# Kernel tuning notes

Hardware: AMD Instinct MI355X
Metric: run time of the kernel (lower is better)

Reference implementation:

```python
import jax, jax.numpy as jnp
import numpy as np

BN_EPS = 1e-5
NUM_GRAPHS = 64


def setup_inputs() -> dict:
    key = jax.random.key(0)
    ks = jax.random.split(key, 16)
    N, E, C_in, H, L, G = 100000, 1600000, 32, 64, 4, NUM_GRAPHS
    x = jax.random.normal(ks[0], (N, C_in), dtype=jnp.float32)
    edge_index = jax.random.randint(ks[1], (2, E), 0, N, dtype=jnp.int64)
    batch = jnp.sort(jax.random.randint(ks[2], (N,), 0, G, dtype=jnp.int64))
    s_in = 1.0 / np.sqrt(C_in)
    s_h = 1.0 / np.sqrt(H)
    s_2h = 1.0 / np.sqrt(2 * H)
    Win = jax.random.uniform(ks[3], (C_in, H), jnp.float32, -s_in, s_in)
    bin_ = jax.random.uniform(ks[4], (H,), jnp.float32, -s_in, s_in)
    W1s = jax.random.uniform(ks[5], (L, H, 2 * H), jnp.float32, -s_h, s_h)
    b1s = jax.random.uniform(ks[6], (L, 2 * H), jnp.float32, -s_h, s_h)
    gammas = jnp.ones((L, 2 * H), jnp.float32)
    betas = jnp.zeros((L, 2 * H), jnp.float32)
    W2s = jax.random.uniform(ks[7], (L, 2 * H, H), jnp.float32, -s_2h, s_2h)
    b2s = jax.random.uniform(ks[8], (L, H), jnp.float32, -s_2h, s_2h)
    epss = jnp.zeros((L,), jnp.float32)
    Wout = jax.random.uniform(ks[9], (H, 1), jnp.float32, -s_h, s_h)
    bout = jax.random.uniform(ks[10], (1,), jnp.float32, -s_h, s_h)
    return {"x": x, "edge_index": edge_index, "batch": batch, "Win": Win,
            "bin_": bin_, "W1s": W1s, "b1s": b1s, "gammas": gammas,
            "betas": betas, "W2s": W2s, "b2s": b2s, "epss": epss,
            "Wout": Wout, "bout": bout}


def _gin_layer(x, src, dst, W1, b1, gamma, beta, W2, b2, eps, n_nodes):
    # message: relu of source node features; aggregate: scatter-add at target
    agg = jax.ops.segment_sum(jax.nn.relu(x[src]), dst, num_segments=n_nodes)
    h = (1.0 + eps) * x + agg
    h = h @ W1 + b1
    mu = jnp.mean(h, axis=0)
    var = jnp.mean(jnp.square(h - mu), axis=0)  # biased, as in BatchNorm1d
    h = (h - mu) * jax.lax.rsqrt(var + BN_EPS) * gamma + beta
    h = jax.nn.relu(h)
    return h @ W2 + b2


def reference(x, edge_index, batch, Win, bin_, W1s, b1s, gammas, betas,
              W2s, b2s, epss, Wout, bout):
    N = x.shape[0]
    src, dst = edge_index[0], edge_index[1]
    x = x @ Win + bin_
    for l in range(W1s.shape[0]):
        x = x + _gin_layer(x, src, dst, W1s[l], b1s[l], gammas[l], betas[l],
                           W2s[l], b2s[l], epss[l], N)
    pooled = jax.ops.segment_sum(x, batch, num_segments=NUM_GRAPHS)  # [G, H]
    out = pooled @ Wout + bout
    return out.reshape(-1)
```

## Files before the change

### kernel.cpp

```cpp
#include <hip/hip_runtime.h>
#include <hip/hip_fp16.h>

#define H 64
#define CIN 32
#define TWOH 128
#define NGRAPH 64

#define BSH 7
#define BNODE 128
#define NBLK_PART 256
#define BCAP 32
#define MAXNB 2048
#define OCAP 65536

typedef unsigned short bfraw;
typedef short v8s __attribute__((ext_vector_type(8)));
typedef float v4f __attribute__((ext_vector_type(4)));

__device__ __forceinline__ float bf2f(bfraw u) {
    return __uint_as_float(((unsigned)u) << 16);
}
__device__ __forceinline__ bfraw f2bf(float f) {
    unsigned u = __float_as_uint(f);
    unsigned r = (u + 0x7fffu + ((u >> 16) & 1u)) >> 16;
    return (bfraw)r;
}
__device__ __forceinline__ void f2bf2(float f, bfraw& hi, bfraw& lo) {
    hi = f2bf(f);
    lo = f2bf(f - bf2f(hi));
}
__device__ __forceinline__ bfraw f2h(float f) {
    return __half_as_ushort(__float2half(f));
}
__device__ __forceinline__ __half2 u2h2(unsigned u) {
    union { unsigned u; __half2 h; } c; c.u = u; return c.h;
}

extern "C" __global__ void __launch_bounds__(256) k_input_gemm(
    const float* __restrict__ x, const float* __restrict__ Win,
    const float* __restrict__ bin, float* __restrict__ x0,
    bfraw* __restrict__ xh, int N)
{
    const int lane = threadIdx.x & 63;
    const int row = lane & 15;
    const int kg  = lane >> 4;
    v8s bhi[4], blo[4];
    #pragma unroll
    for (int ct = 0; ct < 4; ++ct) {
        v8s bh, bl;
        #pragma unroll
        for (int i = 0; i < 8; ++i) {
            const float w = Win[(kg * 8 + i) * H + ct * 16 + row];
            bfraw h, l; f2bf2(w, h, l);
            bh[i] = (short)h; bl[i] = (short)l;
        }
        bhi[ct] = bh; blo[ct] = bl;
    }
    float bcol[4];
    #pragma unroll
    for (int ct = 0; ct < 4; ++ct) bcol[ct] = bin[ct * 16 + row];

    const int wpb = blockDim.x >> 6;
    const int wid = blockIdx.x * wpb + (threadIdx.x >> 6);
    const int wstride = gridDim.x * wpb;
    const int tiles = (N + 15) >> 4;
    for (int t = wid; t < tiles; t += wstride) {
        const int tb = t << 4;
        int nA = tb + row; if (nA >= N) nA = N - 1;
        v8s ah, al;
        #pragma unroll
        for (int i = 0; i < 8; ++i) {
            const float v = x[(size_t)nA * CIN + kg * 8 + i];
            bfraw h, l; f2bf2(v, h, l);
            ah[i] = (short)h; al[i] = (short)l;
        }
        v4f c[4];
        #pragma unroll
        for (int ct = 0; ct < 4; ++ct) {
            v4f cc = (v4f){0.f, 0.f, 0.f, 0.f};
            cc = __builtin_amdgcn_mfma_f32_16x16x32_bf16(ah, bhi[ct], cc, 0, 0, 0);
            cc = __builtin_amdgcn_mfma_f32_16x16x32_bf16(ah, blo[ct], cc, 0, 0, 0);
            cc = __builtin_amdgcn_mfma_f32_16x16x32_bf16(al, bhi[ct], cc, 0, 0, 0);
            c[ct] = cc;
        }
        #pragma unroll
        for (int ct = 0; ct < 4; ++ct) {
            #pragma unroll
            for (int r = 0; r < 4; ++r) {
                const int node = tb + kg * 4 + r;
                if (node < N) {
                    const float v = c[ct][r] + bcol[ct];
                    const size_t idx = (size_t)node * H + ct * 16 + row;
                    x0[idx] = v;
                    xh[idx] = f2h(fmaxf(v, 0.f));
                }
            }
        }
    }
}

extern "C" __global__ void k_cvtw(const float* __restrict__ W1s,
    const float* __restrict__ W2s, bfraw* __restrict__ W1hi,
    bfraw* __restrict__ W1lo, bfraw* __restrict__ W2hi,
    bfraw* __restrict__ W2lo, int total)
{
    int i = blockIdx.x * blockDim.x + threadIdx.x;
    const int st = gridDim.x * blockDim.x;
    for (; i < total; i += st) {
        bfraw h, l;
        f2bf2(W1s[i], h, l); W1hi[i] = h; W1lo[i] = l;
        f2bf2(W2s[i], h, l); W2hi[i] = h; W2lo[i] = l;
    }
}

__device__ __forceinline__ void bput(int s, int d, unsigned* __restrict__ lcnt,
    unsigned* __restrict__ myTmp, unsigned* __restrict__ deg,
    int* __restrict__ oflow, unsigned* __restrict__ ocnt)
{
    const int b = d >> BSH;
    const unsigned pos = atomicAdd(&lcnt[b], 1u);
    if (pos < BCAP) {
        myTmp[b * BCAP + pos] = (unsigned)s | ((unsigned)(d & (BNODE - 1)) << 20);
    } else {
        const unsigned o = atomicAdd(ocnt, 1u);
        if (o < OCAP) {
            oflow[2 * o] = s; oflow[2 * o + 1] = d;
            atomicAdd(&deg[d], 1u);
        }
    }
}

extern "C" __global__ void __launch_bounds__(256) k_bucket(
    const int* __restrict__ src, const int* __restrict__ dst,
    unsigned* __restrict__ bcnt, unsigned* __restrict__ btmp,
    unsigned* __restrict__ deg, int* __restrict__ oflow,
    unsigned* __restrict__ ocnt, int E, int NBck)
{
    __shared__ unsigned lcnt[MAXNB];
    for (int i = threadIdx.x; i < NBck; i += blockDim.x) lcnt[i] = 0u;
    __syncthreads();
    unsigned* __restrict__ myTmp = btmp + (size_t)blockIdx.x * NBck * BCAP;
    const int tid0 = blockIdx.x * blockDim.x + threadIdx.x;
    const int st = gridDim.x * blockDim.x;
    const int E4 = E >> 2;
    const int4* s4 = (const int4*)src;
    const int4* d4 = (const int4*)dst;
    for (int j = tid0; j < E4; j += st) {
        const int4 sv = s4[j];
        const int4 dv = d4[j];
        bput(sv.x, dv.x, lcnt, myTmp, deg, oflow, ocnt);
        bput(sv.y, dv.y, lcnt, myTmp, deg, oflow, ocnt);
        bput(sv.z, dv.z, lcnt, myTmp, deg, oflow, ocnt);
        bput(sv.w, dv.w, lcnt, myTmp, deg, oflow, ocnt);
    }
    for (int j = (E4 << 2) + tid0; j < E; j += st)
        bput(src[j], dst[j], lcnt, myTmp, deg, oflow, ocnt);
    __syncthreads();
    unsigned* __restrict__ myCnt = bcnt + (size_t)blockIdx.x * NBck;
    for (int i = threadIdx.x; i < NBck; i += blockDim.x) {
        const unsigned c = lcnt[i];
        myCnt[i] = (c < BCAP) ? c : BCAP;
    }
}

extern "C" __global__ void __launch_bounds__(256) k_bhist(
    const unsigned* __restrict__ bcnt, const unsigned* __restrict__ btmp,
    unsigned* __restrict__ deg, int N, int NBck)
{
    __shared__ unsigned hist[BNODE];
    const int b = blockIdx.x;
    for (int i = threadIdx.x; i < BNODE; i += blockDim.x) hist[i] = 0u;
    __syncthreads();
    for (int blk = threadIdx.x; blk < NBLK_PART; blk += blockDim.x) {
        const unsigned cnt = bcnt[(size_t)blk * NBck + b];
        const unsigned* p = btmp + ((size_t)blk * NBck + b) * BCAP;
        for (unsigned j = 0; j < cnt; ++j)
            atomicAdd(&hist[p[j] >> 20], 1u);
    }
    __syncthreads();
    const int base = b << BSH;
    for (int i = threadIdx.x; i < BNODE; i += blockDim.x)
        if (base + i < N) {
            const unsigned h = hist[i];
            if (h) atomicAdd(&deg[base + i], h);
        }
}

extern "C" __global__ void k_scan1(const unsigned* __restrict__ deg,
    unsigned* __restrict__ indptr, unsigned* __restrict__ bsum, int N)
{
    __shared__ unsigned s[256];
    const int tid = threadIdx.x;
    const int base = blockIdx.x * 1024 + tid * 4;
    unsigned d[4];
    #pragma unroll
    for (int j = 0; j < 4; ++j)
        d[j] = (base + j < N) ? ((deg[base + j] + 7u) & ~7u) : 0u;
    unsigned t = d[0] + d[1] + d[2] + d[3];
    s[tid] = t;
    __syncthreads();
    for (int o = 1; o < 256; o <<= 1) {
        unsigned v = (tid >= o) ? s[tid - o] : 0u;
        __syncthreads();
        s[tid] += v;
        __syncthreads();
    }
    unsigned run = (tid == 0) ? 0u : s[tid - 1];
    if (tid == 255) bsum[blockIdx.x] = s[255];
    #pragma unroll
    for (int j = 0; j < 4; ++j) {
        if (base + j < N) indptr[base + j] = run;
        run += d[j];
    }
}

extern "C" __global__ void k_scan2(unsigned* bsum, int nb,
    unsigned* __restrict__ indptr, int N)
{
    if (threadIdx.x == 0) {
        unsigned run = 0;
        for (int i = 0; i < nb; ++i) { unsigned v = bsum[i]; bsum[i] = run; run += v; }
        indptr[N] = run;
    }
}

extern "C" __global__ void k_scan3(unsigned* __restrict__ indptr,
    const unsigned* __restrict__ bsum, unsigned* __restrict__ cursor, int N)
{
    const int base = blockIdx.x * 1024 + threadIdx.x * 4;
    const unsigned boff = bsum[blockIdx.x];
    #pragma unroll
    for (int j = 0; j < 4; ++j) {
        const int idx = base + j;
        if (idx < N) {
            const unsigned v = indptr[idx] + boff;
            indptr[idx] = v;
            cursor[idx] = v;
        }
    }
}

extern "C" __global__ void __launch_bounds__(256) k_bscat(
    const unsigned* __restrict__ bcnt, const unsigned* __restrict__ btmp,
    const unsigned* __restrict__ indptr, unsigned* __restrict__ cursor,
    int* __restrict__ esrc, int N, int NBck)
{
    __shared__ unsigned lcur[BNODE];
    const int b = blockIdx.x;
    const int base = b << BSH;
    for (int i = threadIdx.x; i < BNODE; i += blockDim.x)
        lcur[i] = (base + i < N) ? indptr[base + i] : 0u;
    __syncthreads();
    for (int blk = threadIdx.x; blk < NBLK_PART; blk += blockDim.x) {
        const unsigned cnt = bcnt[(size_t)blk * NBck + b];
        const unsigned* p = btmp + ((size_t)blk * NBck + b) * BCAP;
        for (unsigned j = 0; j < cnt; ++j) {
            const unsigned e = p[j];
            const unsigned pos = atomicAdd(&lcur[e >> 20], 1u);
            esrc[pos] = (int)(e & 0xFFFFFu);
        }
    }
    __syncthreads();
    for (int i = threadIdx.x; i < BNODE; i += blockDim.x)
        if (base + i < N) cursor[base + i] = lcur[i];
}

extern "C" __global__ void k_over(const int* __restrict__ oflow,
    const unsigned* __restrict__ ocnt, unsigned* __restrict__ cursor,
    int* __restrict__ esrc)
{
    unsigned n = *ocnt; if (n > OCAP) n = OCAP;
    int i = blockIdx.x * blockDim.x + threadIdx.x;
    const int st = gridDim.x * blockDim.x;
    for (; (unsigned)i < n; i += st) {
        const int s = oflow[2 * i], d = oflow[2 * i + 1];
        const unsigned pos = atomicAdd(&cursor[d], 1u);
        esrc[pos] = s;
    }
}

extern "C" __global__ void k_pad(const unsigned* __restrict__ cursor,
    const unsigned* __restrict__ indptr, int* __restrict__ esrc, int N)
{
    int n = blockIdx.x * blockDim.x + threadIdx.x;
    const int st = gridDim.x * blockDim.x;
    for (; n < N; n += st) {
        const unsigned end = indptr[n + 1];
        for (unsigned p = cursor[n]; p < end; ++p) esrc[p] = N;
    }
}

extern "C" __global__ void __launch_bounds__(256) k_agg(
    const float* __restrict__ x0, const bfraw* __restrict__ xh,
    const int* __restrict__ esrc, const unsigned* __restrict__ indptr,
    const float* __restrict__ epsp, bfraw* __restrict__ hprehi,
    bfraw* __restrict__ hprelo, int N)
{
    const int lane = threadIdx.x & 63;
    const int sub = lane >> 4;
    const int fi = (lane & 15) << 2;
    const int wpb = blockDim.x >> 6;
    int w = blockIdx.x * wpb + (threadIdx.x >> 6);
    const int wstride = gridDim.x * wpb;
    const float ep = 1.f + epsp[0];
    for (int n = w; n < N; n += wstride) {
        const unsigned s0 = indptr[n];
        const unsigned s1 = indptr[n + 1];
        float a0 = 0.f, a1 = 0.f, a2 = 0.f, a3 = 0.f;
        unsigned e = s0;
        for (; e + 16 <= s1; e += 16) {
            int idx[4];
            #pragma unroll
            for (int j = 0; j < 4; ++j) idx[j] = esrc[e + 4 * j + sub];
            uint2 r[4];
            #pragma unroll
            for (int j = 0; j < 4; ++j)
                r[j] = *(const uint2*)&xh[(size_t)idx[j] * H + fi];
            const __half2 s01 = __hadd2(__hadd2(u2h2(r[0].x), u2h2(r[1].x)),
                                        __hadd2(u2h2(r[2].x), u2h2(r[3].x)));
            const __half2 s23 = __hadd2(__hadd2(u2h2(r[0].y), u2h2(r[1].y)),
                                        __hadd2(u2h2(r[2].y), u2h2(r[3].y)));
            const float2 f01 = __half22float2(s01);
            const float2 f23 = __half22float2(s23);
            a0 += f01.x; a1 += f01.y; a2 += f23.x; a3 += f23.y;
        }
        for (; e + 8 <= s1; e += 8) {
            const int i0 = esrc[e + sub];
            const int i1 = esrc[e + 4 + sub];
            const uint2 r0 = *(const uint2*)&xh[(size_t)i0 * H + fi];
            const uint2 r1 = *(const uint2*)&xh[(size_t)i1 * H + fi];
            const float2 f01 = __half22float2(__hadd2(u2h2(r0.x), u2h2(r1.x)));
            const float2 f23 = __half22float2(__hadd2(u2h2(r0.y), u2h2(r1.y)));
            a0 += f01.x; a1 += f01.y; a2 += f23.x; a3 += f23.y;
        }
        for (; e < s1; e += 4) {
            const int i0 = esrc[e + sub];
            const uint2 r = *(const uint2*)&xh[(size_t)i0 * H + fi];
            const float2 f01 = __half22float2(u2h2(r.x));
            const float2 f23 = __half22float2(u2h2(r.y));
            a0 += f01.x; a1 += f01.y; a2 += f23.x; a3 += f23.y;
        }
        #pragma unroll
        for (int o = 16; o < 64; o <<= 1) {
            a0 += __shfl_xor(a0, o);
            a1 += __shfl_xor(a1, o);
            a2 += __shfl_xor(a2, o);
            a3 += __shfl_xor(a3, o);
        }
        if (sub == 0) {
            const float4 self = *(const float4*)&x0[(size_t)n * H + fi];
            const float h0 = ep * self.x + a0;
            const float h1v = ep * self.y + a1;
            const float h2 = ep * self.z + a2;
            const float h3 = ep * self.w + a3;
            ushort4 ohi, olo;
            f2bf2(h0, ohi.x, olo.x);
            f2bf2(h1v, ohi.y, olo.y);
            f2bf2(h2, ohi.z, olo.z);
            f2bf2(h3, ohi.w, olo.w);
            *(ushort4*)&hprehi[(size_t)n * H + fi] = ohi;
            *(ushort4*)&hprelo[(size_t)n * H + fi] = olo;
        }
    }
}

extern "C" __global__ void __launch_bounds__(256) k_gemm1(
    const bfraw* __restrict__ hprehi, const bfraw* __restrict__ hprelo,
    const bfraw* __restrict__ W1hi, const bfraw* __restrict__ W1lo,
    const float* __restrict__ b1, float* __restrict__ h1,
    double* __restrict__ gsum, double* __restrict__ gsq, int N)
{
    __shared__ float ss[TWOH], sq[TWOH];
    if (threadIdx.x < TWOH) { ss[threadIdx.x] = 0.f; sq[threadIdx.x] = 0.f; }
    __syncthreads();
    const int lane = threadIdx.x & 63;
    const int row = lane & 15;
    const int kg  = lane >> 4;
    const int wpb = blockDim.x >> 6;
    const int wid = blockIdx.x * wpb + (threadIdx.x >> 6);
    const int wstride = gridDim.x * wpb;
    const int half = wid & 1;
    const int cb = half * 4;
    v8s bhi[2][4], blo[2][4];
    #pragma unroll
    for (int kc = 0; kc < 2; ++kc)
        #pragma unroll
        for (int ct = 0; ct < 4; ++ct) {
            v8s bh, bl;
            #pragma unroll
            for (int i = 0; i < 8; ++i) {
                const int idx = (kc * 32 + kg * 8 + i) * TWOH + (cb + ct) * 16 + row;
                bh[i] = (short)W1hi[idx];
                bl[i] = (short)W1lo[idx];
            }
            bhi[kc][ct] = bh; blo[kc][ct] = bl;
        }
    float bcol[4];
    #pragma unroll
    for (int ct = 0; ct < 4; ++ct) bcol[ct] = b1[(cb + ct) * 16 + row];

    const int tiles = (N + 15) >> 4;
    const int tstride = wstride >> 1;
    float sacc[4], qacc[4];
    #pragma unroll
    for (int ct = 0; ct < 4; ++ct) { sacc[ct] = 0.f; qacc[ct] = 0.f; }

    for (int t = wid >> 1; t < tiles; t += tstride) {
        const int tb = t << 4;
        int nA = tb + row; if (nA >= N) nA = N - 1;
        const v8s a0h = *(const v8s*)&hprehi[(size_t)nA * H + kg * 8];
        const v8s a1h = *(const v8s*)&hprehi[(size_t)nA * H + 32 + kg * 8];
        const v8s a0l = *(const v8s*)&hprelo[(size_t)nA * H + kg * 8];
        const v8s a1l = *(const v8s*)&hprelo[(size_t)nA * H + 32 + kg * 8];
        v4f c[4];
        #pragma unroll
        for (int ct = 0; ct < 4; ++ct) {
            v4f cc = (v4f){0.f, 0.f, 0.f, 0.f};
            cc = __builtin_amdgcn_mfma_f32_16x16x32_bf16(a0h, bhi[0][ct], cc, 0, 0, 0);
            cc = __builtin_amdgcn_mfma_f32_16x16x32_bf16(a1h, bhi[1][ct], cc, 0, 0, 0);
            cc = __builtin_amdgcn_mfma_f32_16x16x32_bf16(a0h, blo[0][ct], cc, 0, 0, 0);
            cc = __builtin_amdgcn_mfma_f32_16x16x32_bf16(a1h, blo[1][ct], cc, 0, 0, 0);
            cc = __builtin_amdgcn_mfma_f32_16x16x32_bf16(a0l, bhi[0][ct], cc, 0, 0, 0);
            cc = __builtin_amdgcn_mfma_f32_16x16x32_bf16(a1l, bhi[1][ct], cc, 0, 0, 0);
            c[ct] = cc;
        }
        #pragma unroll
        for (int ct = 0; ct < 4; ++ct) {
            #pragma unroll
            for (int r = 0; r < 4; ++r) {
                const int node = tb + kg * 4 + r;
                if (node < N) {
                    const float v = c[ct][r] + bcol[ct];
                    h1[(size_t)node * TWOH + (cb + ct) * 16 + row] = v;
                    sacc[ct] += v;
                    qacc[ct] += v * v;
                }
            }
        }
    }
    #pragma unroll
    for (int ct = 0; ct < 4; ++ct) {
        float s = sacc[ct];
        s += __shfl_xor(s, 16); s += __shfl_xor(s, 32);
        float q = qacc[ct];
        q += __shfl_xor(q, 16); q += __shfl_xor(q, 32);
        if (kg == 0) {
            atomicAdd(&ss[(cb + ct) * 16 + row], s);
            atomicAdd(&sq[(cb + ct) * 16 + row], q);
        }
    }
    __syncthreads();
    if (threadIdx.x < TWOH) {
        atomicAdd(&gsum[threadIdx.x], (double)ss[threadIdx.x]);
        atomicAdd(&gsq[threadIdx.x], (double)sq[threadIdx.x]);
    }
}

extern "C" __global__ void k_bnfin(const double* __restrict__ gsum,
    const double* __restrict__ gsq, const float* __restrict__ gamma,
    const float* __restrict__ beta, float* __restrict__ scsh, int N)
{
    const int j = threadIdx.x;
    if (j < TWOH) {
        const double mu = gsum[j] / N;
        const double var = gsq[j] / N - mu * mu;
        const float sc = gamma[j] * rsqrtf(fmaxf((float)var, 0.f) + 1e-5f);
        scsh[j] = sc;
        scsh[TWOH + j] = beta[j] - (float)mu * sc;
    }
}

extern "C" __global__ void __launch_bounds__(256) k_gemm2(
    const float* __restrict__ h1, const float* __restrict__ scsh,
    const bfraw* __restrict__ W2hi, const bfraw* __restrict__ W2lo,
    const float* __restrict__ b2, float* __restrict__ x0,
    bfraw* __restrict__ xh, int N)
{
    __shared__ float scl[TWOH], shl[TWOH];
    for (int i = threadIdx.x; i < TWOH; i += blockDim.x) {
        scl[i] = scsh[i];
        shl[i] = scsh[TWOH + i];
    }
    __syncthreads();
    const int lane = threadIdx.x & 63;
    const int row = lane & 15;
    const int kg  = lane >> 4;
    const int wpb = blockDim.x >> 6;
    const int wid = blockIdx.x * wpb + (threadIdx.x >> 6);
    const int wstride = gridDim.x * wpb;
    const int half = wid & 1;
    const int cb = half * 2;
    v8s bhi[4][2], blo[4][2];
    #pragma unroll
    for (int kc = 0; kc < 4; ++kc)
        #pragma unroll
        for (int ct = 0; ct < 2; ++ct) {
            v8s bh, bl;
            #pragma unroll
            for (int i = 0; i < 8; ++i) {
                const int idx = (kc * 32 + kg * 8 + i) * H + (cb + ct) * 16 + row;
                bh[i] = (short)W2hi[idx];
                bl[i] = (short)W2lo[idx];
            }
            bhi[kc][ct] = bh; blo[kc][ct] = bl;
        }
    float bcol[2];
    #pragma unroll
    for (int ct = 0; ct < 2; ++ct) bcol[ct] = b2[(cb + ct) * 16 + row];
    float lsc[4][8], lsh[4][8];
    #pragma unroll
    for (int kc = 0; kc < 4; ++kc) {
        const int fb = kc * 32 + kg * 8;
        #pragma unroll
        for (int i = 0; i < 8; ++i) { lsc[kc][i] = scl[fb + i]; lsh[kc][i] = shl[fb + i]; }
    }

    const int tiles = (N + 15) >> 4;
    const int tstride = wstride >> 1;

    for (int t = wid >> 1; t < tiles; t += tstride) {
        const int tb = t << 4;
        int nA = tb + row; if (nA >= N) nA = N - 1;
        v8s ah[4], al[4];
        #pragma unroll
        for (int kc = 0; kc < 4; ++kc) {
            const int fb = kc * 32 + kg * 8;
            const float4 h0 = *(const float4*)&h1[(size_t)nA * TWOH + fb];
            const float4 h4 = *(const float4*)&h1[(size_t)nA * TWOH + fb + 4];
            float yv[8] = {h0.x, h0.y, h0.z, h0.w, h4.x, h4.y, h4.z, h4.w};
            v8s vh, vl;
            #pragma unroll
            for (int i = 0; i < 8; ++i) {
                const float y = fmaxf(yv[i] * lsc[kc][i] + lsh[kc][i], 0.f);
                bfraw hi, lo;
                f2bf2(y, hi, lo);
                vh[i] = (short)hi;
                vl[i] = (short)lo;
            }
            ah[kc] = vh; al[kc] = vl;
        }
        v4f c[2];
        #pragma unroll
        for (int ct = 0; ct < 2; ++ct) {
            v4f cc = (v4f){0.f, 0.f, 0.f, 0.f};
            #pragma unroll
            for (int kc = 0; kc < 4; ++kc) {
                cc = __builtin_amdgcn_mfma_f32_16x16x32_bf16(ah[kc], bhi[kc][ct], cc, 0, 0, 0);
                cc = __builtin_amdgcn_mfma_f32_16x16x32_bf16(ah[kc], blo[kc][ct], cc, 0, 0, 0);
                cc = __builtin_amdgcn_mfma_f32_16x16x32_bf16(al[kc], bhi[kc][ct], cc, 0, 0, 0);
            }
            c[ct] = cc;
        }
        #pragma unroll
        for (int ct = 0; ct < 2; ++ct) {
            #pragma unroll
            for (int r = 0; r < 4; ++r) {
                const int node = tb + kg * 4 + r;
                if (node < N) {
                    const size_t idx = (size_t)node * H + (cb + ct) * 16 + row;
                    const float v = x0[idx] + c[ct][r] + bcol[ct];
                    x0[idx] = v;
                    xh[idx] = f2h(fmaxf(v, 0.f));
                }
            }
        }
    }
}

extern "C" __global__ void k_initout(const float* __restrict__ bout,
    float* __restrict__ out)
{
    if (threadIdx.x < NGRAPH) out[threadIdx.x] = bout[0];
}

extern "C" __global__ void __launch_bounds__(256) k_pool(
    const float* __restrict__ x0, const int* __restrict__ batch,
    const float* __restrict__ Wout, float* __restrict__ out, int N)
{
    const int lane = threadIdx.x & 63;
    const int wpb = blockDim.x >> 6;
    const int gw = blockIdx.x * wpb + (threadIdx.x >> 6);
    const int nw = gridDim.x * wpb;
    const int per = (N + nw - 1) / nw;
    const int n0 = gw * per;
    int n1 = n0 + per; if (n1 > N) n1 = N;
    if (n0 >= N) return;
    const float wv = Wout[lane];
    int cur = batch[n0];
    float acc = 0.f;
    for (int n = n0; n < n1; ++n) {
        const int g = batch[n];
        if (g != cur) {
            float v = acc * wv;
            #pragma unroll
            for (int o = 32; o > 0; o >>= 1) v += __shfl_down(v, o);
            if (lane == 0) atomicAdd(&out[cur], v);
            cur = g;
            acc = 0.f;
        }
        acc += x0[(size_t)n * H + lane];
    }
    float v = acc * wv;
    #pragma unroll
    for (int o = 32; o > 0; o >>= 1) v += __shfl_down(v, o);
    if (lane == 0) atomicAdd(&out[cur], v);
}

extern "C" void kernel_launch(void* const* d_in, const int* in_sizes, int n_in,
                              void* d_out, int out_size, void* d_ws, size_t ws_size,
                              hipStream_t stream)
{
    const float* x     = (const float*)d_in[0];
    const int*   ei    = (const int*)d_in[1];
    const int*   batch = (const int*)d_in[2];
    const float* Win   = (const float*)d_in[3];
    const float* bin   = (const float*)d_in[4];
    const float* W1s   = (const float*)d_in[5];
    const float* b1s   = (const float*)d_in[6];
    const float* gam   = (const float*)d_in[7];
    const float* bet   = (const float*)d_in[8];
    const float* W2s   = (const float*)d_in[9];
    const float* b2s   = (const float*)d_in[10];
    const float* epss  = (const float*)d_in[11];
    const float* Wout  = (const float*)d_in[12];
    const float* bout  = (const float*)d_in[13];

    const int N = in_sizes[0] / CIN;
    const int E = in_sizes[1] / 2;
    const int L = in_sizes[11];
    const int* src = ei;
    const int* dst = ei + E;
    const int NB = (N + BNODE - 1) >> BSH;

    char* ws = (char*)d_ws;
    size_t off = 0;
    auto take = [&](size_t bytes) {
        void* p = ws + off;
        off += (bytes + 255) & ~(size_t)255;
        return p;
    };
    float*    x0     = (float*)take((size_t)N * H * 4);
    bfraw*    xh     = (bfraw*)take((size_t)(N + 1) * H * 2);
    bfraw*    hprehi = (bfraw*)take((size_t)N * H * 2);
    bfraw*    hprelo = (bfraw*)take((size_t)N * H * 2);
    float*    h1     = (float*)take((size_t)N * TWOH * 4);
    unsigned* deg    = (unsigned*)take((size_t)N * 4);
    unsigned* indptr = (unsigned*)take((size_t)(N + 1) * 4);
    unsigned* cursor = (unsigned*)take((size_t)N * 4);
    int*      esrc   = (int*)take((size_t)(E + 8 * (N + 1)) * 4);
    unsigned* bsum   = (unsigned*)take(4096);
    double*   gsum   = (double*)take(TWOH * 8 * 2);
    double*   gsq    = gsum + TWOH;
    float*    scsh   = (float*)take(2 * TWOH * 4);
    bfraw*    W1hi   = (bfraw*)take((size_t)L * H * TWOH * 2);
    bfraw*    W1lo   = (bfraw*)take((size_t)L * H * TWOH * 2);
    bfraw*    W2hi   = (bfraw*)take((size_t)L * TWOH * H * 2);
    bfraw*    W2lo   = (bfraw*)take((size_t)L * TWOH * H * 2);
    unsigned* bcnt   = (unsigned*)take((size_t)NBLK_PART * NB * 4);
    unsigned* btmp   = (unsigned*)take((size_t)NBLK_PART * NB * BCAP * 4);
    int*      oflow  = (int*)take((size_t)OCAP * 2 * 4);
    unsigned* ocnt   = (unsigned*)take(256);
    (void)ws_size; (void)n_in; (void)out_size;

    hipMemsetAsync(deg, 0, (size_t)N * 4, stream);
    hipMemsetAsync(ocnt, 0, 4, stream);
    hipMemsetAsync(xh + (size_t)N * H, 0, H * 2, stream);
    k_input_gemm<<<512, 256, 0, stream>>>(x, Win, bin, x0, xh, N);
    k_cvtw<<<256, 256, 0, stream>>>(W1s, W2s, W1hi, W1lo, W2hi, W2lo, L * H * TWOH);
    k_bucket<<<NBLK_PART, 256, 0, stream>>>(src, dst, bcnt, btmp, deg, oflow, ocnt, E, NB);
    k_bhist<<<NB, 256, 0, stream>>>(bcnt, btmp, deg, N, NB);
    const int nb = (N + 1023) / 1024;
    k_scan1<<<nb, 256, 0, stream>>>(deg, indptr, bsum, N);
    k_scan2<<<1, 64, 0, stream>>>(bsum, nb, indptr, N);
    k_scan3<<<nb, 256, 0, stream>>>(indptr, bsum, cursor, N);
    k_bscat<<<NB, 256, 0, stream>>>(bcnt, btmp, indptr, cursor, esrc, N, NB);
    k_over<<<32, 256, 0, stream>>>(oflow, ocnt, cursor, esrc);
    k_pad<<<512, 256, 0, stream>>>(cursor, indptr, esrc, N);

    for (int l = 0; l < L; ++l) {
        hipMemsetAsync(gsum, 0, TWOH * 8 * 2, stream);
        k_agg<<<4096, 256, 0, stream>>>(x0, xh, esrc, indptr, epss + l,
            hprehi, hprelo, N);
        k_gemm1<<<512, 256, 0, stream>>>(hprehi, hprelo,
            W1hi + (size_t)l * H * TWOH, W1lo + (size_t)l * H * TWOH,
            b1s + (size_t)l * TWOH, h1, gsum, gsq, N);
        k_bnfin<<<1, 128, 0, stream>>>(gsum, gsq, gam + (size_t)l * TWOH,
            bet + (size_t)l * TWOH, scsh, N);
        k_gemm2<<<512, 256, 0, stream>>>(h1, scsh,
            W2hi + (size_t)l * TWOH * H, W2lo + (size_t)l * TWOH * H,
            b2s + (size_t)l * H, x0, xh, N);
    }

    k_initout<<<1, 64, 0, stream>>>(bout, (float*)d_out);
    k_pool<<<512, 256, 0, stream>>>(x0, batch, Wout, (float*)d_out, N);
}
```

Measured before the change: 518.9 us.

## Switch split-bf16 MFMA to fp16 with fp16 activations and intermediates

Replaces the three-term hi/lo bf16 MFMA emulation of fp32 with fp16 MFMAs: activations are held as a single fp16 value and weights keep an fp16 hi/lo split, so each product needs two MFMAs instead of three. The pre-activation buffer now stores one fp16 array instead of hi and lo bf16 arrays, and the 128-wide hidden activation h1 is stored in fp16 rather than fp32, roughly halving that buffer's traffic. The intent is to cut both MFMA count and memory bandwidth across the per-layer kernels. The cost is lower precision, since activations are rounded to fp16 with its limited range and mantissa, including before the batch-norm normalisation.

```diff
diff --git a/kernel.cpp b/kernel.cpp
--- a/kernel.cpp
+++ b/kernel.cpp
@@ -14,26 +14,24 @@
 #define OCAP 65536
 
 typedef unsigned short bfraw;
-typedef short v8s __attribute__((ext_vector_type(8)));
+typedef _Float16 v8h __attribute__((ext_vector_type(8)));
+typedef unsigned short v8u __attribute__((ext_vector_type(8)));
 typedef float v4f __attribute__((ext_vector_type(4)));
 
-__device__ __forceinline__ float bf2f(bfraw u) {
-    return __uint_as_float(((unsigned)u) << 16);
-}
-__device__ __forceinline__ bfraw f2bf(float f) {
-    unsigned u = __float_as_uint(f);
-    unsigned r = (u + 0x7fffu + ((u >> 16) & 1u)) >> 16;
-    return (bfraw)r;
-}
-__device__ __forceinline__ void f2bf2(float f, bfraw& hi, bfraw& lo) {
-    hi = f2bf(f);
-    lo = f2bf(f - bf2f(hi));
-}
+union h8cast { v8u u; v8h h; uint4 q; };
+
 __device__ __forceinline__ bfraw f2h(float f) {
     return __half_as_ushort(__float2half(f));
 }
+__device__ __forceinline__ float h2f(bfraw u) {
+    return __half2float(__ushort_as_half(u));
+}
 __device__ __forceinline__ __half2 u2h2(unsigned u) {
     union { unsigned u; __half2 h; } c; c.u = u; return c.h;
+}
+__device__ __forceinline__ void f2h2(float f, _Float16& hi, _Float16& lo) {
+    hi = (_Float16)f;
+    lo = (_Float16)(f - (float)hi);
 }
 
 extern "C" __global__ void __launch_bounds__(256) k_input_gemm(
@@ -44,15 +42,15 @@
     const int lane = threadIdx.x & 63;
     const int row = lane & 15;
     const int kg  = lane >> 4;
-    v8s bhi[4], blo[4];
+    v8h bhi[4], blo[4];
     #pragma unroll
     for (int ct = 0; ct < 4; ++ct) {
-        v8s bh, bl;
+        v8h bh, bl;
         #pragma unroll
         for (int i = 0; i < 8; ++i) {
             const float w = Win[(kg * 8 + i) * H + ct * 16 + row];
-            bfraw h, l; f2bf2(w, h, l);
-            bh[i] = (short)h; bl[i] = (short)l;
+            _Float16 h, l; f2h2(w, h, l);
+            bh[i] = h; bl[i] = l;
         }
         bhi[ct] = bh; blo[ct] = bl;
     }
@@ -67,20 +65,16 @@
     for (int t = wid; t < tiles; t += wstride) {
         const int tb = t << 4;
         int nA = tb + row; if (nA >= N) nA = N - 1;
-        v8s ah, al;
-        #pragma unroll
-        for (int i = 0; i < 8; ++i) {
-            const float v = x[(size_t)nA * CIN + kg * 8 + i];
-            bfraw h, l; f2bf2(v, h, l);
-            ah[i] = (short)h; al[i] = (short)l;
-        }
+        v8h a;
+        #pragma unroll
+        for (int i = 0; i < 8; ++i)
+            a[i] = (_Float16)x[(size_t)nA * CIN + kg * 8 + i];
         v4f c[4];
         #pragma unroll
         for (int ct = 0; ct < 4; ++ct) {
             v4f cc = (v4f){0.f, 0.f, 0.f, 0.f};
-            cc = __builtin_amdgcn_mfma_f32_16x16x32_bf16(ah, bhi[ct], cc, 0, 0, 0);
-            cc = __builtin_amdgcn_mfma_f32_16x16x32_bf16(ah, blo[ct], cc, 0, 0, 0);
-            cc = __builtin_amdgcn_mfma_f32_16x16x32_bf16(al, bhi[ct], cc, 0, 0, 0);
+            cc = __builtin_amdgcn_mfma_f32_16x16x32_f16(a, bhi[ct], cc, 0, 0, 0);
+            cc = __builtin_amdgcn_mfma_f32_16x16x32_f16(a, blo[ct], cc, 0, 0, 0);
             c[ct] = cc;
         }
         #pragma unroll
@@ -107,9 +101,18 @@
     int i = blockIdx.x * blockDim.x + threadIdx.x;
     const int st = gridDim.x * blockDim.x;
     for (; i < total; i += st) {
-        bfraw h, l;
-        f2bf2(W1s[i], h, l); W1hi[i] = h; W1lo[i] = l;
-        f2bf2(W2s[i], h, l); W2hi[i] = h; W2lo[i] = l;
+        {
+            const float w = W1s[i];
+            const bfraw hb = f2h(w);
+            W1hi[i] = hb;
+            W1lo[i] = f2h(w - h2f(hb));
+        }
+        {
+            const float w = W2s[i];
+            const bfraw hb = f2h(w);
+            W2hi[i] = hb;
+            W2lo[i] = f2h(w - h2f(hb));
+        }
     }
 }
 
@@ -293,8 +296,7 @@
 extern "C" __global__ void __launch_bounds__(256) k_agg(
     const float* __restrict__ x0, const bfraw* __restrict__ xh,
     const int* __restrict__ esrc, const unsigned* __restrict__ indptr,
-    const float* __restrict__ epsp, bfraw* __restrict__ hprehi,
-    bfraw* __restrict__ hprelo, int N)
+    const float* __restrict__ epsp, bfraw* __restrict__ hpreh, int N)
 {
     const int lane = threadIdx.x & 63;
     const int sub = lane >> 4;
@@ -349,25 +351,20 @@
         }
         if (sub == 0) {
             const float4 self = *(const float4*)&x0[(size_t)n * H + fi];
-            const float h0 = ep * self.x + a0;
-            const float h1v = ep * self.y + a1;
-            const float h2 = ep * self.z + a2;
-            const float h3 = ep * self.w + a3;
-            ushort4 ohi, olo;
-            f2bf2(h0, ohi.x, olo.x);
-            f2bf2(h1v, ohi.y, olo.y);
-            f2bf2(h2, ohi.z, olo.z);
-            f2bf2(h3, ohi.w, olo.w);
-            *(ushort4*)&hprehi[(size_t)n * H + fi] = ohi;
-            *(ushort4*)&hprelo[(size_t)n * H + fi] = olo;
+            ushort4 o;
+            o.x = f2h(ep * self.x + a0);
+            o.y = f2h(ep * self.y + a1);
+            o.z = f2h(ep * self.z + a2);
+            o.w = f2h(ep * self.w + a3);
+            *(ushort4*)&hpreh[(size_t)n * H + fi] = o;
         }
     }
 }
 
 extern "C" __global__ void __launch_bounds__(256) k_gemm1(
-    const bfraw* __restrict__ hprehi, const bfraw* __restrict__ hprelo,
+    const bfraw* __restrict__ hpreh,
     const bfraw* __restrict__ W1hi, const bfraw* __restrict__ W1lo,
-    const float* __restrict__ b1, float* __restrict__ h1,
+    const float* __restrict__ b1, bfraw* __restrict__ h1h,
     double* __restrict__ gsum, double* __restrict__ gsq, int N)
 {
     __shared__ float ss[TWOH], sq[TWOH];
@@ -381,17 +378,17 @@
     const int wstride = gridDim.x * wpb;
     const int half = wid & 1;
     const int cb = half * 4;
-    v8s bhi[2][4], blo[2][4];
+    v8h bhi[2][4], blo[2][4];
     #pragma unroll
     for (int kc = 0; kc < 2; ++kc)
         #pragma unroll
         for (int ct = 0; ct < 4; ++ct) {
-            v8s bh, bl;
+            v8h bh, bl;
             #pragma unroll
             for (int i = 0; i < 8; ++i) {
                 const int idx = (kc * 32 + kg * 8 + i) * TWOH + (cb + ct) * 16 + row;
-                bh[i] = (short)W1hi[idx];
-                bl[i] = (short)W1lo[idx];
+                bh[i] = (_Float16)__ushort_as_half(W1hi[idx]);
+                bl[i] = (_Float16)__ushort_as_half(W1lo[idx]);
             }
             bhi[kc][ct] = bh; blo[kc][ct] = bl;
         }
@@ -408,20 +405,19 @@
     for (int t = wid >> 1; t < tiles; t += tstride) {
         const int tb = t << 4;
         int nA = tb + row; if (nA >= N) nA = N - 1;
-        const v8s a0h = *(const v8s*)&hprehi[(size_t)nA * H + kg * 8];
-        const v8s a1h = *(const v8s*)&hprehi[(size_t)nA * H + 32 + kg * 8];
-        const v8s a0l = *(const v8s*)&hprelo[(size_t)nA * H + kg * 8];
-        const v8s a1l = *(const v8s*)&hprelo[(size_t)nA * H + 32 + kg * 8];
+        h8cast a0c, a1c;
+        a0c.q = *(const uint4*)&hpreh[(size_t)nA * H + kg * 8];
+        a1c.q = *(const uint4*)&hpreh[(size_t)nA * H + 32 + kg * 8];
+        const v8h a0 = a0c.h;
+        const v8h a1 = a1c.h;
         v4f c[4];
         #pragma unroll
         for (int ct = 0; ct < 4; ++ct) {
             v4f cc = (v4f){0.f, 0.f, 0.f, 0.f};
-            cc = __builtin_amdgcn_mfma_f32_16x16x32_bf16(a0h, bhi[0][ct], cc, 0, 0, 0);
-            cc = __builtin_amdgcn_mfma_f32_16x16x32_bf16(a1h, bhi[1][ct], cc, 0, 0, 0);
-            cc = __builtin_amdgcn_mfma_f32_16x16x32_bf16(a0h, blo[0][ct], cc, 0, 0, 0);
-            cc = __builtin_amdgcn_mfma_f32_16x16x32_bf16(a1h, blo[1][ct], cc, 0, 0, 0);
-            cc = __builtin_amdgcn_mfma_f32_16x16x32_bf16(a0l, bhi[0][ct], cc, 0, 0, 0);
-            cc = __builtin_amdgcn_mfma_f32_16x16x32_bf16(a1l, bhi[1][ct], cc, 0, 0, 0);
+            cc = __builtin_amdgcn_mfma_f32_16x16x32_f16(a0, bhi[0][ct], cc, 0, 0, 0);
+            cc = __builtin_amdgcn_mfma_f32_16x16x32_f16(a1, bhi[1][ct], cc, 0, 0, 0);
+            cc = __builtin_amdgcn_mfma_f32_16x16x32_f16(a0, blo[0][ct], cc, 0, 0, 0);
+            cc = __builtin_amdgcn_mfma_f32_16x16x32_f16(a1, blo[1][ct], cc, 0, 0, 0);
             c[ct] = cc;
         }
         #pragma unroll
@@ -431,7 +427,7 @@
                 const int node = tb + kg * 4 + r;
                 if (node < N) {
                     const float v = c[ct][r] + bcol[ct];
-                    h1[(size_t)node * TWOH + (cb + ct) * 16 + row] = v;
+                    h1h[(size_t)node * TWOH + (cb + ct) * 16 + row] = f2h(v);
                     sacc[ct] += v;
                     qacc[ct] += v * v;
                 }
@@ -471,7 +467,7 @@
 }
 
 extern "C" __global__ void __launch_bounds__(256) k_gemm2(
-    const float* __restrict__ h1, const float* __restrict__ scsh,
+    const bfraw* __restrict__ h1h, const float* __restrict__ scsh,
     const bfraw* __restrict__ W2hi, const bfraw* __restrict__ W2lo,
     const float* __restrict__ b2, float* __restrict__ x0,
     bfraw* __restrict__ xh, int N)
@@ -490,17 +486,17 @@
     const int wstride = gridDim.x * wpb;
     const int half = wid & 1;
     const int cb = half * 2;
-    v8s bhi[4][2], blo[4][2];
+    v8h bhi[4][2], blo[4][2];
     #pragma unroll
     for (int kc = 0; kc < 4; ++kc)
         #pragma unroll
         for (int ct = 0; ct < 2; ++ct) {
-            v8s bh, bl;
+            v8h bh, bl;
             #pragma unroll
             for (int i = 0; i < 8; ++i) {
                 const int idx = (kc * 32 + kg * 8 + i) * H + (cb + ct) * 16 + row;
-                bh[i] = (short)W2hi[idx];
-                bl[i] = (short)W2lo[idx];
+                bh[i] = (_Float16)__ushort_as_half(W2hi[idx]);
+                bl[i] = (_Float16)__ushort_as_half(W2lo[idx]);
             }
             bhi[kc][ct] = bh; blo[kc][ct] = bl;
         }
@@ -521,23 +517,19 @@
     for (int t = wid >> 1; t < tiles; t += tstride) {
         const int tb = t << 4;
         int nA = tb + row; if (nA >= N) nA = N - 1;
-        v8s ah[4], al[4];
+        v8h a[4];
         #pragma unroll
         for (int kc = 0; kc < 4; ++kc) {
             const int fb = kc * 32 + kg * 8;
-            const float4 h0 = *(const float4*)&h1[(size_t)nA * TWOH + fb];
-            const float4 h4 = *(const float4*)&h1[(size_t)nA * TWOH + fb + 4];
-            float yv[8] = {h0.x, h0.y, h0.z, h0.w, h4.x, h4.y, h4.z, h4.w};
-            v8s vh, vl;
+            h8cast hc;
+            hc.q = *(const uint4*)&h1h[(size_t)nA * TWOH + fb];
+            v8h va;
             #pragma unroll
             for (int i = 0; i < 8; ++i) {
-                const float y = fmaxf(yv[i] * lsc[kc][i] + lsh[kc][i], 0.f);
-                bfraw hi, lo;
-                f2bf2(y, hi, lo);
-                vh[i] = (short)hi;
-                vl[i] = (short)lo;
+                const float hv = (float)hc.h[i];
+                va[i] = (_Float16)fmaxf(hv * lsc[kc][i] + lsh[kc][i], 0.f);
             }
-            ah[kc] = vh; al[kc] = vl;
+            a[kc] = va;
         }
         v4f c[2];
         #pragma unroll
@@ -545,9 +537,8 @@
             v4f cc = (v4f){0.f, 0.f, 0.f, 0.f};
             #pragma unroll
             for (int kc = 0; kc < 4; ++kc) {
-                cc = __builtin_amdgcn_mfma_f32_16x16x32_bf16(ah[kc], bhi[kc][ct], cc, 0, 0, 0);
-                cc = __builtin_amdgcn_mfma_f32_16x16x32_bf16(ah[kc], blo[kc][ct], cc, 0, 0, 0);
-                cc = __builtin_amdgcn_mfma_f32_16x16x32_bf16(al[kc], bhi[kc][ct], cc, 0, 0, 0);
+                cc = __builtin_amdgcn_mfma_f32_16x16x32_f16(a[kc], bhi[kc][ct], cc, 0, 0, 0);
+                cc = __builtin_amdgcn_mfma_f32_16x16x32_f16(a[kc], blo[kc][ct], cc, 0, 0, 0);
             }
             c[ct] = cc;
         }
@@ -641,9 +632,8 @@
     };
     float*    x0     = (float*)take((size_t)N * H * 4);
     bfraw*    xh     = (bfraw*)take((size_t)(N + 1) * H * 2);
-    bfraw*    hprehi = (bfraw*)take((size_t)N * H * 2);
-    bfraw*    hprelo = (bfraw*)take((size_t)N * H * 2);
-    float*    h1     = (float*)take((size_t)N * TWOH * 4);
+    bfraw*    hpreh  = (bfraw*)take((size_t)N * H * 2);
+    bfraw*    h1h    = (bfraw*)take((size_t)N * TWOH * 2);
     unsigned* deg    = (unsigned*)take((size_t)N * 4);
     unsigned* indptr = (unsigned*)take((size_t)(N + 1) * 4);
     unsigned* cursor = (unsigned*)take((size_t)N * 4);
@@ -679,14 +669,13 @@
 
     for (int l = 0; l < L; ++l) {
         hipMemsetAsync(gsum, 0, TWOH * 8 * 2, stream);
-        k_agg<<<4096, 256, 0, stream>>>(x0, xh, esrc, indptr, epss + l,
-            hprehi, hprelo, N);
-        k_gemm1<<<512, 256, 0, stream>>>(hprehi, hprelo,
+        k_agg<<<4096, 256, 0, stream>>>(x0, xh, esrc, indptr, epss + l, hpreh, N);
+        k_gemm1<<<512, 256, 0, stream>>>(hpreh,
             W1hi + (size_t)l * H * TWOH, W1lo + (size_t)l * H * TWOH,
-            b1s + (size_t)l * TWOH, h1, gsum, gsq, N);
+            b1s + (size_t)l * TWOH, h1h, gsum, gsq, N);
         k_bnfin<<<1, 128, 0, stream>>>(gsum, gsq, gam + (size_t)l * TWOH,
             bet + (size_t)l * TWOH, scsh, N);
-        k_gemm2<<<512, 256, 0, stream>>>(h1, scsh,
+        k_gemm2<<<512, 256, 0, stream>>>(h1h, scsh,
             W2hi + (size_t)l * TWOH * H, W2lo + (size_t)l * TWOH * H,
             b2s + (size_t)l * H, x0, xh, N);
     }
```

New measurement: 469.2 us. -9.6%, faster.
